# Kernel tuning notes

Measured on AMD Instinct MI355X. Metric: run time of the kernel, lower is better.

## Reference

```python
import jax, jax.numpy as jnp
import numpy as np

B, N, D = 2, 2048, 128
DEPTH, RECURRENCE = 3, 3
EDGE_P = 0.03  # Bernoulli edge density -> avg degree ~61


def _p(key, shape, fan_in):
    return jax.random.normal(key, shape, dtype=jnp.float32) / np.float32(np.sqrt(fan_in))


def setup_inputs() -> dict:
    key = jax.random.key(0)
    ks = jax.random.split(key, 6)
    node = jax.random.normal(ks[0], (B, N, 1), dtype=jnp.float32)
    A = (jax.random.uniform(ks[1], (B, N, N)) < EDGE_P).astype(jnp.float32)
    edge = jax.random.uniform(ks[2], (B, N, N), dtype=jnp.float32) + 0.1  # strictly positive edge weights
    inp = {"node": node, "edge": edge, "A": A}
    # (fan_in, heads) per attention layer; last layer hardcodes heads=2, concat=False
    specs = [(1, 1), (D, 1), (D, 2)]
    for l, (fin, H) in enumerate(specs):
        kk = jax.random.split(ks[3 + l], 5)
        inp[f"Wq{l}"] = _p(kk[0], (fin, H, D), fin)
        inp[f"Wk{l}"] = _p(kk[1], (fin, H, D), fin)
        inp[f"Wv{l}"] = _p(kk[2], (fin, H, D), fin)
        inp[f"We{l}"] = _p(kk[3], (H, D), 1)  # lin_edge: edge_dim=1 -> H*D, stored as (H, D)
        inp[f"Ws{l}"] = _p(kk[4], (fin, H * D if l < DEPTH - 1 else D), fin)  # root/skip lin
    return inp


def _layer_norm(x, eps=1e-5):
    mu = x.mean(-1, keepdims=True)
    var = ((x - mu) ** 2).mean(-1, keepdims=True)
    return (x - mu) / jnp.sqrt(var + eps)


def _tconv(x, e_t, mask, Wq, Wk, Wv, We, Ws, concat):
    # PyG TransformerConv (bias removed, root_weight=True):
    #   alpha_ij = softmax_j( q_i . (k_j + W_e e_ij) / sqrt(d) ) over in-neighbors j of i
    #   out_i = sum_j alpha_ij (v_j + W_e e_ij)  (+ W_skip x_i)
    # e_ij is a scalar so W_e e_ij = e_ij * We, a rank-1 term we never materialize per-edge.
    # x: (b,n,fin); e_t[b,dst,src]; We: (H,d)
    H, d = We.shape
    q = jnp.einsum('bnf,fhd->bnhd', x, Wq)
    k = jnp.einsum('bnf,fhd->bnhd', x, Wk)
    v = jnp.einsum('bnf,fhd->bnhd', x, Wv)
    scores = jnp.einsum('bihd,bjhd->bhij', q, k)  # i=dst, j=src
    qe = jnp.einsum('bihd,hd->bhi', q, We)
    scores = (scores + qe[..., None] * e_t[:, None]) / np.float32(np.sqrt(d))
    scores = jnp.where(mask[:, None], scores, jnp.finfo(scores.dtype).min)
    alpha = jax.nn.softmax(scores, axis=-1)
    alpha = jnp.where(mask[:, None], alpha, 0.0)  # isolated dst nodes aggregate to zero
    out = jnp.einsum('bhij,bjhd->bihd', alpha, v)
    ew = jnp.einsum('bhij,bij->bhi', alpha, e_t)  # sum_j alpha * e_ij
    out = out + ew.transpose(0, 2, 1)[..., None] * We
    out = out.reshape(x.shape[0], x.shape[1], H * d) if concat else out.mean(axis=2)
    return out + x @ Ws


def reference(node, edge, A, Wq0, Wk0, Wv0, We0, Ws0, Wq1, Wk1, Wv1, We1, Ws1, Wq2, Wk2, Wv2, We2, Ws2):
    e = edge * A
    e_t = jnp.swapaxes(e, 1, 2)  # e_t[b, dst, src]  (edge_index: row=src, col=dst)
    mask = e_t != 0  # dense_to_sparse keeps nonzero entries
    layers = [
        (Wq0, Wk0, Wv0, We0, Ws0, True),
        (Wq1, Wk1, Wv1, We1, Ws1, True),
        (Wq2, Wk2, Wv2, We2, Ws2, False),
    ]
    emb = node
    for r in range(RECURRENCE):
        for l in range(DEPTH):
            if r != 0 and l == 0:
                continue
            Wq, Wk, Wv, We, Ws, concat = layers[l]
            emb = _tconv(emb, e_t, mask, Wq, Wk, Wv, We, Ws, concat)
            if l != DEPTH - 1:
                emb = jax.nn.relu(_layer_norm(emb))
    return emb  # (b, n, out_dim[-1])
```

## Files before the change

### kernel.cpp

```cpp
#include <hip/hip_runtime.h>
#include <hip/hip_bf16.h>

#define BB 2
#define NN 2048
#define DD 128
#define BN (BB*NN)
#define CAP 128
#define TD 32
#define QSTR 256
#define SSTR 128
#define INV_SQRT_D 0.08838834764831845f

typedef __attribute__((ext_vector_type(8))) short short8;
typedef __attribute__((ext_vector_type(4))) float f32x4;

__device__ inline float b2f(unsigned short u) {
    union { unsigned int i; float f; } c; c.i = (unsigned int)u << 16; return c.f;
}
__device__ inline float b2f_hi(unsigned int raw) {
    union { unsigned int i; float f; } c; c.i = raw & 0xffff0000u; return c.f;
}
__device__ inline float b2f_lo(unsigned int raw) {
    union { unsigned int i; float f; } c; c.i = raw << 16; return c.f;
}

__device__ inline float dpp_sum16(float x) {
    int v;
    v = __builtin_bit_cast(int, x);
    x += __builtin_bit_cast(float, __builtin_amdgcn_update_dpp(0, v, 0xB1,  0xF, 0xF, true));
    v = __builtin_bit_cast(int, x);
    x += __builtin_bit_cast(float, __builtin_amdgcn_update_dpp(0, v, 0x4E,  0xF, 0xF, true));
    v = __builtin_bit_cast(int, x);
    x += __builtin_bit_cast(float, __builtin_amdgcn_update_dpp(0, v, 0x124, 0xF, 0xF, true));
    v = __builtin_bit_cast(int, x);
    x += __builtin_bit_cast(float, __builtin_amdgcn_update_dpp(0, v, 0x128, 0xF, 0xF, true));
    return x;
}

__device__ inline float readlane_f(float x, int l) {
    return __builtin_bit_cast(float, __builtin_amdgcn_readlane(__builtin_bit_cast(int, x), l));
}

__global__ __launch_bounds__(256) void prep(
    const float* __restrict__ A, const float* __restrict__ edge,
    const float* __restrict__ node,
    const float* __restrict__ Wq0, const float* __restrict__ Wk0,
    const float* __restrict__ Wv0, const float* __restrict__ Ws0,
    const float* __restrict__ Wq1, const float* __restrict__ Wk1,
    const float* __restrict__ Wv1, const float* __restrict__ Ws1,
    const float* __restrict__ Wq2, const float* __restrict__ Wk2,
    const float* __restrict__ Wv2, const float* __restrict__ Ws2,
    __hip_bfloat16* __restrict__ Wt1, __hip_bfloat16* __restrict__ Wt2,
    float* __restrict__ q, __hip_bfloat16* __restrict__ kA,
    __hip_bfloat16* __restrict__ vA, float* __restrict__ s,
    int* __restrict__ deg, unsigned short* __restrict__ cols,
    float* __restrict__ evals)
{
    __shared__ int   cnt[TD];
    __shared__ int   wbase[TD];
    __shared__ int   csh[TD][CAP];
    __shared__ float esh[TD][CAP];
    __shared__ float xnode[16];

    int bid = blockIdx.x;
    int tid = threadIdx.x;

    if (bid < 1024) {
        int b     = bid >> 9;
        int r     = bid & 511;
        int dst0  = (r >> 3) * TD;
        int chunk = r & 7;

        if (tid < TD) cnt[tid] = 0;
        __syncthreads();

        int srcOff = tid >> 3;
        int dOff   = (tid & 7) * 4;
        int src0   = chunk * 256;
        const size_t base = (size_t)b * NN * NN + (size_t)src0 * NN + dst0 + dOff;

#pragma unroll 2
        for (int s0 = 0; s0 < 256; s0 += 32) {
            int srel = s0 + srcOff;
            float4 a4 = *(const float4*)&A[base + (size_t)srel * NN];
            float4 e4 = *(const float4*)&edge[base + (size_t)srel * NN];
            int gsrc = b * NN + src0 + srel;
            float av[4] = {a4.x, a4.y, a4.z, a4.w};
            float ev[4] = {e4.x, e4.y, e4.z, e4.w};
#pragma unroll
            for (int u = 0; u < 4; u++) {
                if (av[u] != 0.f) {
                    int d = dOff + u;
                    int slot = atomicAdd(&cnt[d], 1);
                    if (slot < CAP) { csh[d][slot] = gsrc; esh[d][slot] = ev[u] * av[u]; }
                }
            }
        }
        __syncthreads();

        if (tid < TD) {
            int c = min(cnt[tid], CAP);
            cnt[tid] = c;
            wbase[tid] = atomicAdd(&deg[b * NN + dst0 + tid], c);
        }
        __syncthreads();

        for (int idx = tid; idx < TD * CAP; idx += 256) {
            int d = idx >> 7, i = idx & 127;
            if (i < cnt[d]) {
                int slot = wbase[d] + i;
                if (slot < CAP) {
                    size_t row = (size_t)(b * NN + dst0 + d);
                    cols [row * CAP + slot] = (unsigned short)csh[d][i];
                    evals[row * CAP + slot] = esh[d][i];
                }
            }
        }
    } else if (bid < 1024 + 1408) {
        int c = bid - 1024;
        if (tid < DD) {
            const float *Wq, *Wk, *Wv, *Ws; __hip_bfloat16* Wt; int n, HD;
            if (c < 512) { Wq = Wq1; Wk = Wk1; Wv = Wv1; Ws = Ws1; Wt = Wt1; n = c;       HD = DD;     }
            else         { Wq = Wq2; Wk = Wk2; Wv = Wv2; Ws = Ws2; Wt = Wt2; n = c - 512; HD = 2 * DD; }
            const float* src; int ld; int col;
            if      (n < HD)     { src = Wq; col = n;          ld = HD; }
            else if (n < 2*HD)   { src = Wk; col = n - HD;     ld = HD; }
            else if (n < 3*HD)   { src = Wv; col = n - 2*HD;   ld = HD; }
            else                 { src = Ws; col = n - 3*HD;   ld = DD; }
            Wt[(size_t)n * DD + tid] = __float2bfloat16(src[(size_t)tid * ld + col]);
        }
    } else {
        int row0 = (bid - (1024 + 1408)) * 16;
        if (tid < 16) xnode[tid] = node[row0 + tid];
        __syncthreads();
        for (int i = tid; i < 16 * 512; i += 256) {
            int r = i >> 9, col = i & 511;
            float xv = xnode[r];
            if (col < DD) {
                q[(size_t)(row0 + r) * QSTR + col] = xv * Wq0[col];
            } else if (col < 2*DD) {
                int lc = col - DD;
                kA[(size_t)(row0 + r) * 256 + lc] = __float2bfloat16(xv * Wk0[lc]);
            } else if (col < 3*DD) {
                int lc = col - 2*DD;
                vA[(size_t)(row0 + r) * 256 + lc] = __float2bfloat16(xv * Wv0[lc]);
            } else {
                int lc = col - 3*DD;
                s[(size_t)(row0 + r) * SSTR + lc] = xv * Ws0[lc];
            }
        }
    }
}

template<int H, int MINW, bool MEANH, bool LNRELU, int NCOLS, int HDN, int KVSI, int KVSO>
__global__ __launch_bounds__(1024, MINW) void fused_attn(
    float* qio,
    const __hip_bfloat16* __restrict__ k,
    const __hip_bfloat16* __restrict__ v,
    float* sio,
    const int* __restrict__ deg,
    const unsigned short* __restrict__ cols,
    const float* __restrict__ evals, const float* __restrict__ We,
    const __hip_bfloat16* __restrict__ Wt,
    __hip_bfloat16* __restrict__ kn, __hip_bfloat16* __restrict__ vn,
    float* __restrict__ out)
{
    const int HD = H * DD;
    constexpr unsigned KROWB = (unsigned)(KVSI * 2);
    int wid  = threadIdx.x >> 6;
    int lane = threadIdx.x & 63;
    int row0 = blockIdx.x * 16;
    int row  = row0 + wid;
    int sub  = lane >> 4;
    int s    = lane & 15;
    int c0   = lane * 2;

    __shared__ int            jc_s[16][CAP];
    __shared__ float          ev_s[16][CAP];
    __shared__ __hip_bfloat16 xs[16][136];
    int*   jc = jc_s[wid];
    float* ev = ev_s[wid];

    int dg = min(deg[row], CAP);
    for (int m = lane; m < dg; m += 64) {
        jc[m] = (int)cols[(size_t)row * CAP + m];
        ev[m] = evals[(size_t)row * CAP + m];
    }
    int dgp = (dg + 7) & ~7;
    if (lane == 0 && dg > 0) {
        int jf = jc[0];
        for (int m = dg; m < dgp; m++) { jc[m] = jf; ev[m] = 0.f; }
    }

    const char* kc = (const char*)k;
    const char* vc = (const char*)v;
    const unsigned kLaneOff = (unsigned)(s * 16);
    const unsigned vLaneOff = (unsigned)(c0 * 2);

    float qh[H][8];
    float qeI[H];
#pragma unroll
    for (int h = 0; h < H; h++) {
        const float* qp = &qio[(size_t)row * QSTR + h * DD + s * 8];
        const float* wp = &We[h * DD + s * 8];
        float pe = 0.f;
#pragma unroll
        for (int t = 0; t < 8; t++) { qh[h][t] = qp[t]; pe += qp[t] * wp[t]; }
        qeI[h] = dpp_sum16(pe) * INV_SQRT_D;
    }

    float l_acc[H], ew_acc[H], acc[H][2];
#pragma unroll
    for (int h = 0; h < H; h++) { l_acc[h] = 0.f; ew_acc[h] = 0.f; acc[h][0] = 0.f; acc[h][1] = 0.f; }

    for (int m0 = 0; m0 < dgp; m0 += 8) {
        int   e0  = m0 + sub,  e1 = m0 + 4 + sub;
        bool  ok0 = e0 < dg,   ok1 = e1 < dg;
        float ee0 = ev[e0],    ee1 = ev[e1];

        unsigned ko0 = (unsigned)jc[e0] * KROWB + kLaneOff;
        unsigned ko1 = (unsigned)jc[e1] * KROWB + kLaneOff;

        int4 j4a = *(const int4*)&jc[m0];
        int4 j4b = *(const int4*)&jc[m0 + 4];
        unsigned vo[8] = {
            (unsigned)j4a.x * KROWB + vLaneOff, (unsigned)j4a.y * KROWB + vLaneOff,
            (unsigned)j4a.z * KROWB + vLaneOff, (unsigned)j4a.w * KROWB + vLaneOff,
            (unsigned)j4b.x * KROWB + vLaneOff, (unsigned)j4b.y * KROWB + vLaneOff,
            (unsigned)j4b.z * KROWB + vLaneOff, (unsigned)j4b.w * KROWB + vLaneOff };

        short8 kk0[H], kk1[H];
#pragma unroll
        for (int h = 0; h < H; h++) {
            kk0[h] = *(const short8*)(kc + (size_t)(ko0 + (unsigned)(h * 256)));
            kk1[h] = *(const short8*)(kc + (size_t)(ko1 + (unsigned)(h * 256)));
        }
        unsigned int vraw[H][8];
#pragma unroll
        for (int h = 0; h < H; h++)
#pragma unroll
            for (int es = 0; es < 8; es++)
                vraw[h][es] = *(const unsigned int*)(vc + (size_t)(vo[es] + (unsigned)(h * 256)));

        __builtin_amdgcn_s_setprio(1);
#pragma unroll
        for (int h = 0; h < H; h++) {
            float p0 = qh[h][0]*b2f((unsigned short)kk0[h][0]) + qh[h][1]*b2f((unsigned short)kk0[h][1])
                     + qh[h][2]*b2f((unsigned short)kk0[h][2]) + qh[h][3]*b2f((unsigned short)kk0[h][3])
                     + qh[h][4]*b2f((unsigned short)kk0[h][4]) + qh[h][5]*b2f((unsigned short)kk0[h][5])
                     + qh[h][6]*b2f((unsigned short)kk0[h][6]) + qh[h][7]*b2f((unsigned short)kk0[h][7]);
            float p1 = qh[h][0]*b2f((unsigned short)kk1[h][0]) + qh[h][1]*b2f((unsigned short)kk1[h][1])
                     + qh[h][2]*b2f((unsigned short)kk1[h][2]) + qh[h][3]*b2f((unsigned short)kk1[h][3])
                     + qh[h][4]*b2f((unsigned short)kk1[h][4]) + qh[h][5]*b2f((unsigned short)kk1[h][5])
                     + qh[h][6]*b2f((unsigned short)kk1[h][6]) + qh[h][7]*b2f((unsigned short)kk1[h][7]);
            p0 = dpp_sum16(p0);
            p1 = dpp_sum16(p1);
            float sc0 = ok0 ? (p0 * INV_SQRT_D + qeI[h] * ee0) : -1e30f;
            float sc1 = ok1 ? (p1 * INV_SQRT_D + qeI[h] * ee1) : -1e30f;
            float a0 = __expf(fminf(sc0, 60.f));
            float a1 = __expf(fminf(sc1, 60.f));
            l_acc[h]  += a0 + a1;
            ew_acc[h] += a0 * ee0 + a1 * ee1;
            float al0[4], al1[4];
#pragma unroll
            for (int es = 0; es < 4; es++) {
                al0[es] = readlane_f(a0, es * 16);
                al1[es] = readlane_f(a1, es * 16);
            }
#pragma unroll
            for (int es = 0; es < 4; es++) {
                acc[h][0] += al0[es] * b2f_lo(vraw[h][es]) + al1[es] * b2f_lo(vraw[h][es + 4]);
                acc[h][1] += al0[es] * b2f_hi(vraw[h][es]) + al1[es] * b2f_hi(vraw[h][es + 4]);
            }
        }
        __builtin_amdgcn_s_setprio(0);
    }

    float rh[H][2];
#pragma unroll
    for (int h = 0; h < H; h++) {
        float l  = l_acc[h]  + __shfl_xor(l_acc[h], 16);
        float ew = ew_acc[h] + __shfl_xor(ew_acc[h], 16);
        l  += __shfl_xor(l, 32);
        ew += __shfl_xor(ew, 32);
        float invZ = (l > 0.f) ? 1.f / l : 0.f;
        rh[h][0] = (acc[h][0] + ew * We[h * DD + c0])     * invZ;
        rh[h][1] = (acc[h][1] + ew * We[h * DD + c0 + 1]) * invZ;
    }
    float r0, r1;
    if constexpr (MEANH) {
        r0 = 0.5f * (rh[0][0] + rh[H - 1][0]);
        r1 = 0.5f * (rh[0][1] + rh[H - 1][1]);
    } else {
        r0 = rh[0][0]; r1 = rh[0][1];
    }
    float2 sk = *(const float2*)&sio[(size_t)row * SSTR + c0];
    r0 += sk.x; r1 += sk.y;

    if constexpr (LNRELU) {
        float sum = r0 + r1, sq = r0 * r0 + r1 * r1;
#pragma unroll
        for (int off = 32; off; off >>= 1) { sum += __shfl_xor(sum, off); sq += __shfl_xor(sq, off); }
        float mu  = sum * (1.f / DD);
        float var = sq * (1.f / DD) - mu * mu;
        float rs  = rsqrtf(var + 1e-5f);
        r0 = fmaxf((r0 - mu) * rs, 0.f);
        r1 = fmaxf((r1 - mu) * rs, 0.f);
    }

    if constexpr (NCOLS == 0) {
        float2 res; res.x = r0; res.y = r1;
        *(float2*)&out[(size_t)row * DD + c0] = res;
    } else {
        __hip_bfloat162 o;
        o.x = __float2bfloat16(r0);
        o.y = __float2bfloat16(r1);
        *(__hip_bfloat162*)&xs[wid][c0] = o;
        __syncthreads();

        int m16 = lane & 15, quad = lane >> 4;
        short8 a[4];
#pragma unroll
        for (int ks = 0; ks < 4; ks++)
            a[ks] = *(const short8*)&xs[m16][ks * 32 + quad * 8];

#pragma unroll 1
        for (int tile = wid; tile < NCOLS / 16; tile += 16) {
            int n0 = tile * 16;
            f32x4 pacc = {0.f, 0.f, 0.f, 0.f};
#pragma unroll
            for (int ks = 0; ks < 4; ks++) {
                const short8* bp = (const short8*)&Wt[(size_t)(n0 + m16) * DD + ks * 32 + quad * 8];
                pacc = __builtin_amdgcn_mfma_f32_16x16x32_bf16(a[ks], *bp, pacc, 0, 0, 0);
            }
            if (n0 < HDN) {
#pragma unroll
                for (int r = 0; r < 4; r++)
                    qio[(size_t)(row0 + quad * 4 + r) * QSTR + n0 + m16] = pacc[r];
            } else if (n0 < 2*HDN) {
                int lc = n0 - HDN;
#pragma unroll
                for (int r = 0; r < 4; r++)
                    kn[(size_t)(row0 + quad * 4 + r) * KVSO + lc + m16] = __float2bfloat16(pacc[r]);
            } else if (n0 < 3*HDN) {
                int lc = n0 - 2*HDN;
#pragma unroll
                for (int r = 0; r < 4; r++)
                    vn[(size_t)(row0 + quad * 4 + r) * KVSO + lc + m16] = __float2bfloat16(pacc[r]);
            } else {
                int lc = n0 - 3*HDN;
#pragma unroll
                for (int r = 0; r < 4; r++)
                    sio[(size_t)(row0 + quad * 4 + r) * SSTR + lc + m16] = pacc[r];
            }
        }
    }
}

extern "C" void kernel_launch(void* const* d_in, const int* in_sizes, int n_in,
                              void* d_out, int out_size, void* d_ws, size_t ws_size,
                              hipStream_t stream)
{
    const float* node = (const float*)d_in[0];
    const float* edge = (const float*)d_in[1];
    const float* A    = (const float*)d_in[2];
    const float* Wq[3] = {(const float*)d_in[3],  (const float*)d_in[8],  (const float*)d_in[13]};
    const float* Wk[3] = {(const float*)d_in[4],  (const float*)d_in[9],  (const float*)d_in[14]};
    const float* Wv[3] = {(const float*)d_in[5],  (const float*)d_in[10], (const float*)d_in[15]};
    const float* We[3] = {(const float*)d_in[6],  (const float*)d_in[11], (const float*)d_in[16]};
    const float* Ws[3] = {(const float*)d_in[7],  (const float*)d_in[12], (const float*)d_in[17]};

    char* p = (char*)d_ws;
    float*          q  = (float*)p;          p += (size_t)BN * QSTR * 4;
    float*          s  = (float*)p;          p += (size_t)BN * SSTR * 4;
    __hip_bfloat16* kA = (__hip_bfloat16*)p; p += (size_t)BN * 256 * 2;
    __hip_bfloat16* vA = (__hip_bfloat16*)p; p += (size_t)BN * 256 * 2;
    __hip_bfloat16* kB = (__hip_bfloat16*)p; p += (size_t)BN * 128 * 2;
    __hip_bfloat16* vB = (__hip_bfloat16*)p; p += (size_t)BN * 128 * 2;
    __hip_bfloat16* Wt1 = (__hip_bfloat16*)p; p += (size_t)512 * DD * 2;
    __hip_bfloat16* Wt2 = (__hip_bfloat16*)p; p += (size_t)896 * DD * 2;
    int*            degb = (int*)p;            p += (size_t)BN * 4;
    float*          evb  = (float*)p;          p += (size_t)BN * CAP * 4;
    unsigned short* colb = (unsigned short*)p; p += (size_t)BN * CAP * 2;

    hipMemsetAsync(degb, 0, (size_t)BN * 4, stream);
    prep<<<1024 + 1408 + BN / 16, 256, 0, stream>>>(
        A, edge, node,
        Wq[0], Wk[0], Wv[0], Ws[0],
        Wq[1], Wk[1], Wv[1], Ws[1],
        Wq[2], Wk[2], Wv[2], Ws[2],
        Wt1, Wt2, q, kA, vA, s, degb, colb, evb);

    fused_attn<1, 8, false, true, 512, 128, 256, 128><<<BN / 16, 1024, 0, stream>>>(
        q, kA, vA, s, degb, colb, evb, We[0], Wt1, kB, vB, nullptr);
    fused_attn<1, 8, false, true, 896, 256, 128, 256><<<BN / 16, 1024, 0, stream>>>(
        q, kB, vB, s, degb, colb, evb, We[1], Wt2, kA, vA, nullptr);
    fused_attn<2, 4, true, false, 512, 128, 256, 128><<<BN / 16, 1024, 0, stream>>>(
        q, kA, vA, s, degb, colb, evb, We[2], Wt1, kB, vB, nullptr);
    fused_attn<1, 8, false, true, 896, 256, 128, 256><<<BN / 16, 1024, 0, stream>>>(
        q, kB, vB, s, degb, colb, evb, We[1], Wt2, kA, vA, nullptr);
    fused_attn<2, 4, true, false, 512, 128, 256, 128><<<BN / 16, 1024, 0, stream>>>(
        q, kA, vA, s, degb, colb, evb, We[2], Wt1, kB, vB, nullptr);
    fused_attn<1, 8, false, true, 896, 256, 128, 256><<<BN / 16, 1024, 0, stream>>>(
        q, kB, vB, s, degb, colb, evb, We[1], Wt2, kA, vA, nullptr);
    fused_attn<2, 4, true, false, 0, 0, 256, 0><<<BN / 16, 1024, 0, stream>>>(
        q, kA, vA, s, degb, colb, evb, We[2], nullptr, nullptr, nullptr, (float*)d_out);
}
```

Before: 283.8 us.

## Store per-chunk neighbor segments to drop global atomics and degree memset

```diff
diff --git a/kernel.cpp b/kernel.cpp
--- a/kernel.cpp
+++ b/kernel.cpp
@@ -7,6 +7,7 @@
 #define BN (BB*NN)
 #define CAP 128
 #define TD 32
+#define CCAP 32
 #define QSTR 256
 #define SSTR 128
 #define INV_SQRT_D 0.08838834764831845f
@@ -53,13 +54,13 @@
     __hip_bfloat16* __restrict__ Wt1, __hip_bfloat16* __restrict__ Wt2,
     float* __restrict__ q, __hip_bfloat16* __restrict__ kA,
     __hip_bfloat16* __restrict__ vA, float* __restrict__ s,
-    int* __restrict__ deg, unsigned short* __restrict__ cols,
-    float* __restrict__ evals)
+    unsigned short* __restrict__ degc,
+    unsigned short* __restrict__ colsc,
+    float* __restrict__ evalsc)
 {
     __shared__ int   cnt[TD];
-    __shared__ int   wbase[TD];
-    __shared__ int   csh[TD][CAP];
-    __shared__ float esh[TD][CAP];
+    __shared__ int   csh[TD][CCAP];
+    __shared__ float esh[TD][CCAP];
     __shared__ float xnode[16];
 
     int bid = blockIdx.x;
@@ -92,28 +93,23 @@
                 if (av[u] != 0.f) {
                     int d = dOff + u;
                     int slot = atomicAdd(&cnt[d], 1);
-                    if (slot < CAP) { csh[d][slot] = gsrc; esh[d][slot] = ev[u] * av[u]; }
+                    if (slot < CCAP) { csh[d][slot] = gsrc; esh[d][slot] = ev[u] * av[u]; }
                 }
             }
         }
         __syncthreads();
 
         if (tid < TD) {
-            int c = min(cnt[tid], CAP);
-            cnt[tid] = c;
-            wbase[tid] = atomicAdd(&deg[b * NN + dst0 + tid], c);
-        }
-        __syncthreads();
-
-        for (int idx = tid; idx < TD * CAP; idx += 256) {
-            int d = idx >> 7, i = idx & 127;
-            if (i < cnt[d]) {
-                int slot = wbase[d] + i;
-                if (slot < CAP) {
-                    size_t row = (size_t)(b * NN + dst0 + d);
-                    cols [row * CAP + slot] = (unsigned short)csh[d][i];
-                    evals[row * CAP + slot] = esh[d][i];
-                }
+            int row = b * NN + dst0 + tid;
+            degc[(size_t)row * 8 + chunk] = (unsigned short)min(cnt[tid], CCAP);
+        }
+
+        for (int idx = tid; idx < TD * CCAP; idx += 256) {
+            int d = idx >> 5, i = idx & (CCAP - 1);
+            if (i < min(cnt[d], CCAP)) {
+                size_t seg = ((size_t)(b * NN + dst0 + d) * 8 + chunk) * CCAP;
+                colsc [seg + i] = (unsigned short)csh[d][i];
+                evalsc[seg + i] = esh[d][i];
             }
         }
     } else if (bid < 1024 + 1408) {
@@ -158,9 +154,10 @@
     const __hip_bfloat16* __restrict__ k,
     const __hip_bfloat16* __restrict__ v,
     float* sio,
-    const int* __restrict__ deg,
-    const unsigned short* __restrict__ cols,
-    const float* __restrict__ evals, const float* __restrict__ We,
+    const unsigned short* __restrict__ degc,
+    const unsigned short* __restrict__ colsc,
+    const float* __restrict__ evalsc,
+    const float* __restrict__ We,
     const __hip_bfloat16* __restrict__ Wt,
     __hip_bfloat16* __restrict__ kn, __hip_bfloat16* __restrict__ vn,
     float* __restrict__ out)
@@ -181,10 +178,28 @@
     int*   jc = jc_s[wid];
     float* ev = ev_s[wid];
 
-    int dg = min(deg[row], CAP);
-    for (int m = lane; m < dg; m += 64) {
-        jc[m] = (int)cols[(size_t)row * CAP + m];
-        ev[m] = evals[(size_t)row * CAP + m];
+    int dg;
+    {
+        const unsigned short* dcp = &degc[(size_t)row * 8];
+        int cnt8[8], offs[8], off = 0;
+#pragma unroll
+        for (int c = 0; c < 8; c++) cnt8[c] = (int)dcp[c];
+#pragma unroll
+        for (int c = 0; c < 8; c++) { offs[c] = off; off += cnt8[c]; }
+        dg = min(off, CAP);
+        const size_t segb = (size_t)row * 8 * CCAP;
+#pragma unroll
+        for (int it = 0; it < 4; it++) {
+            int i = it * 64 + lane;
+            int c = i >> 5, m = i & (CCAP - 1);
+            if (m < cnt8[c]) {
+                int d = offs[c] + m;
+                if (d < CAP) {
+                    jc[d] = (int)colsc[segb + c * CCAP + m];
+                    ev[d] = evalsc[segb + c * CCAP + m];
+                }
+            }
+        }
     }
     int dgp = (dg + 7) & ~7;
     if (lane == 0 && dg > 0) {
@@ -379,30 +394,29 @@
     __hip_bfloat16* vB = (__hip_bfloat16*)p; p += (size_t)BN * 128 * 2;
     __hip_bfloat16* Wt1 = (__hip_bfloat16*)p; p += (size_t)512 * DD * 2;
     __hip_bfloat16* Wt2 = (__hip_bfloat16*)p; p += (size_t)896 * DD * 2;
-    int*            degb = (int*)p;            p += (size_t)BN * 4;
-    float*          evb  = (float*)p;          p += (size_t)BN * CAP * 4;
-    unsigned short* colb = (unsigned short*)p; p += (size_t)BN * CAP * 2;
-
-    hipMemsetAsync(degb, 0, (size_t)BN * 4, stream);
+    unsigned short* degc   = (unsigned short*)p; p += (size_t)BN * 8 * 2;
+    unsigned short* colsc  = (unsigned short*)p; p += (size_t)BN * 8 * CCAP * 2;
+    float*          evalsc = (float*)p;          p += (size_t)BN * 8 * CCAP * 4;
+
     prep<<<1024 + 1408 + BN / 16, 256, 0, stream>>>(
         A, edge, node,
         Wq[0], Wk[0], Wv[0], Ws[0],
         Wq[1], Wk[1], Wv[1], Ws[1],
         Wq[2], Wk[2], Wv[2], Ws[2],
-        Wt1, Wt2, q, kA, vA, s, degb, colb, evb);
+        Wt1, Wt2, q, kA, vA, s, degc, colsc, evalsc);
 
     fused_attn<1, 8, false, true, 512, 128, 256, 128><<<BN / 16, 1024, 0, stream>>>(
-        q, kA, vA, s, degb, colb, evb, We[0], Wt1, kB, vB, nullptr);
+        q, kA, vA, s, degc, colsc, evalsc, We[0], Wt1, kB, vB, nullptr);
     fused_attn<1, 8, false, true, 896, 256, 128, 256><<<BN / 16, 1024, 0, stream>>>(
-        q, kB, vB, s, degb, colb, evb, We[1], Wt2, kA, vA, nullptr);
+        q, kB, vB, s, degc, colsc, evalsc, We[1], Wt2, kA, vA, nullptr);
     fused_attn<2, 4, true, false, 512, 128, 256, 128><<<BN / 16, 1024, 0, stream>>>(
-        q, kA, vA, s, degb, colb, evb, We[2], Wt1, kB, vB, nullptr);
+        q, kA, vA, s, degc, colsc, evalsc, We[2], Wt1, kB, vB, nullptr);
     fused_attn<1, 8, false, true, 896, 256, 128, 256><<<BN / 16, 1024, 0, stream>>>(
-        q, kB, vB, s, degb, colb, evb, We[1], Wt2, kA, vA, nullptr);
+        q, kB, vB, s, degc, colsc, evalsc, We[1], Wt2, kA, vA, nullptr);
     fused_attn<2, 4, true, false, 512, 128, 256, 128><<<BN / 16, 1024, 0, stream>>>(
-        q, kA, vA, s, degb, colb, evb, We[2], Wt1, kB, vB, nullptr);
+        q, kA, vA, s, degc, colsc, evalsc, We[2], Wt1, kB, vB, nullptr);
     fused_attn<1, 8, false, true, 896, 256, 128, 256><<<BN / 16, 1024, 0, stream>>>(
-        q, kB, vB, s, degb, colb, evb, We[1], Wt2, kA, vA, nullptr);
+        q, kB, vB, s, degc, colsc, evalsc, We[1], Wt2, kA, vA, nullptr);
     fused_attn<2, 4, true, false, 0, 0, 256, 0><<<BN / 16, 1024, 0, stream>>>(
-        q, kA, vA, s, degb, colb, evb, We[2], nullptr, nullptr, nullptr, (float*)d_out);
-}
+        q, kA, vA, s, degc, colsc, evalsc, We[2], nullptr, nullptr, nullptr, (float*)d_out);
+}
```

Measured after the change: 279.9 us, median of 2. Within noise of the previous version (-1.4%).
